# Kernel optimization log

Measured on AMD Instinct MI355X. Metric: run time of the kernel, lower is better.

## Reference

```python
import jax, jax.numpy as jnp
import numpy as np

N, E, L = 20000, 640000, 2
D_IN, D_H, D_FF = 1546, 128, 512  # in_channels, heads*out_channels, ff_dim
EPS = 1e-5
SLOPE = 0.01  # LeakyReLU default negative slope


def layer_norm(x, g, b):
    m = x.mean(-1, keepdims=True)
    v = ((x - m) ** 2).mean(-1, keepdims=True)
    return (x - m) / jnp.sqrt(v + EPS) * g + b


def setup_inputs() -> dict:
    key = jax.random.key(0)
    ks = iter(jax.random.split(key, 40))
    f32 = jnp.float32
    def w(shape, scale=0.05):
        return jax.random.normal(next(ks), shape, dtype=f32) * scale
    inp = {
        "x": jax.random.normal(next(ks), (N, D_IN), dtype=f32),
        "edge_index": jax.random.randint(next(ks), (2, E), 0, N, dtype=jnp.int64),
        "edge_attr": jax.random.normal(next(ks), (E, D_H), dtype=f32),
        # per-layer TransformerConv params, stacked over L layers
        "Wq": w((L, D_IN, D_H)), "bq": jnp.zeros((L, D_H), f32),
        "Wk": w((L, D_IN, D_H)), "bk": jnp.zeros((L, D_H), f32),
        "Wv": w((L, D_IN, D_H)), "bv": jnp.zeros((L, D_H), f32),
        "Wr": w((L, D_IN, D_H)), "br": jnp.zeros((L, D_H), f32),
        "Whi": w((L, D_IN, D_H)), "Whj": w((L, D_IN, D_H)),
        # per-layer FFMLP params
        "W1": w((L, D_H, D_FF)), "b1": jnp.zeros((L, D_FF), f32),
        "W2": w((L, D_FF, D_H)), "b2": jnp.zeros((L, D_H), f32),
        "g1": jnp.ones((L, D_H), f32), "be1": jnp.zeros((L, D_H), f32),
        "g2": jnp.ones((L, D_H), f32), "be2": jnp.zeros((L, D_H), f32),
        # shared linear 128->1546 and final linear2 1546->128
        "linW": w((D_H, D_IN)), "linb": jnp.zeros((D_IN,), f32),
        "lin2W": w((D_IN, D_H)), "lin2b": jnp.zeros((D_H,), f32),
    }
    return inp


def reference(x, edge_index, edge_attr, Wq, bq, Wk, bk, Wv, bv, Wr, br,
              Whi, Whj, W1, b1, W2, b2, g1, be1, g2, be2,
              linW, linb, lin2W, lin2b):
    src = edge_index[0]  # j (source)
    dst = edge_index[1]  # i (target)
    for l in range(L):
        q = x @ Wq[l] + bq[l]          # [N, D_H]
        k = x @ Wk[l] + bk[l]
        v = x @ Wv[l] + bv[l]
        hi = x @ Whi[l]
        hj = x @ Whj[l]
        # edge gate (uses raw edge_attr, matching original forward)
        gate = jax.nn.sigmoid(edge_attr + hi[src] + hj[dst])      # [E, D_H]
        # per-edge scalar attention, softmax over ALL edges (dim=0, as in source)
        attn = jnp.sum(q[dst] * k[src], axis=-1, keepdims=True)   # [E, 1]
        attn = jax.nn.softmax(attn, axis=0)
        msg = attn * v[src] * gate                                 # [E, D_H]
        aggr = jax.ops.segment_sum(msg, dst, num_segments=N)       # [N, D_H]
        h = aggr + x @ Wr[l] + br[l]   # root weight, concat=False -> no out_proj
        # FFMLP (pre-norm residual on normalized input)
        ss = layer_norm(h, g1[l], be1[l])
        ss2 = jax.nn.relu(ss @ W1[l] + b1[l]) @ W2[l] + b2[l]
        h = layer_norm(ss + ss2, g2[l], be2[l])
        x = h @ linW + linb            # shared 128 -> 1546
    x = jax.nn.leaky_relu(x @ lin2W + lin2b, SLOPE)
    return x
```

## Files before the change

### kernel.cpp

```cpp
#include <hip/hip_runtime.h>
#include <cfloat>
#include <cmath>

#define NN 20000
#define EE 640000
#define DIN 1546
#define KIN 1568
#define DH 128
#define DFF 512
#define NL 2
#define NPROJ 768
#define NB (NN / 4)

typedef unsigned short ushort_t;
typedef __attribute__((ext_vector_type(8))) short short8;
typedef __attribute__((ext_vector_type(8))) unsigned short ushort8;
typedef __attribute__((ext_vector_type(4))) float floatx4;

__device__ inline ushort_t f2bf(float f) {
  unsigned u = __float_as_uint(f);
  unsigned r = (u + 0x7FFF + ((u >> 16) & 1)) >> 16;
  return (ushort_t)r;
}
__device__ inline float bflo(unsigned u) { return __uint_as_float(u << 16); }
__device__ inline float bfhi(unsigned u) { return __uint_as_float(u & 0xFFFF0000u); }

__global__ __launch_bounds__(256) void gemm_bf16(
    const ushort_t* __restrict__ A, int lda,
    const ushort_t* __restrict__ Bt, int ldb,
    const float* __restrict__ bias, void* __restrict__ Cv, int ldc,
    int M, int Nstore, int K, int act, int out_bf16)
{
  __shared__ ushort_t As[4 * 1032];
  __shared__ ushort_t Bs[4 * 1032];
  const int tid = threadIdx.x;
  const int wave = tid >> 6, lane = tid & 63;
  const int bm = blockIdx.x * 128, bn = blockIdx.y * 128;
  const int wm = (wave >> 1) * 64, wn = (wave & 1) * 64;
  const int frow = lane & 15, kq = lane >> 4;

  floatx4 acc[4][4];
  #pragma unroll
  for (int i = 0; i < 4; ++i)
    #pragma unroll
    for (int j = 0; j < 4; ++j) acc[i][j] = (floatx4){0.f, 0.f, 0.f, 0.f};

  const int srow = tid >> 2, skc = tid & 3;
  const int ar0 = min(bm + srow, M - 1);
  const int ar1 = min(bm + srow + 64, M - 1);
  const ushort_t* Ap0 = A + (size_t)ar0 * lda + skc * 8;
  const ushort_t* Ap1 = A + (size_t)ar1 * lda + skc * 8;
  const ushort_t* Bp0 = Bt + (size_t)(bn + srow) * ldb + skc * 8;
  const ushort_t* Bp1 = Bt + (size_t)(bn + srow + 64) * ldb + skc * 8;
  ushort_t* Aw0 = As + skc * 1032 + srow * 8;
  ushort_t* Aw1 = As + skc * 1032 + (srow + 64) * 8;
  ushort_t* Bw0 = Bs + skc * 1032 + srow * 8;
  ushort_t* Bw1 = Bs + skc * 1032 + (srow + 64) * 8;

  for (int k0 = 0; k0 < K; k0 += 32) {
    ushort8 a0 = *(const ushort8*)Ap0; Ap0 += 32;
    ushort8 a1 = *(const ushort8*)Ap1; Ap1 += 32;
    ushort8 b0 = *(const ushort8*)Bp0; Bp0 += 32;
    ushort8 b1 = *(const ushort8*)Bp1; Bp1 += 32;
    __syncthreads();
    *(ushort8*)Aw0 = a0; *(ushort8*)Aw1 = a1;
    *(ushort8*)Bw0 = b0; *(ushort8*)Bw1 = b1;
    __syncthreads();
    short8 af[4], bfv[4];
    #pragma unroll
    for (int i = 0; i < 4; ++i)
      af[i] = *(const short8*)(As + kq * 1032 + (wm + i * 16 + frow) * 8);
    #pragma unroll
    for (int j = 0; j < 4; ++j)
      bfv[j] = *(const short8*)(Bs + kq * 1032 + (wn + j * 16 + frow) * 8);
    #pragma unroll
    for (int i = 0; i < 4; ++i)
      #pragma unroll
      for (int j = 0; j < 4; ++j)
        acc[i][j] = __builtin_amdgcn_mfma_f32_16x16x32_bf16(af[i], bfv[j], acc[i][j], 0, 0, 0);
  }

  const int rq = (lane >> 4) * 4;
  #pragma unroll
  for (int j = 0; j < 4; ++j) {
    int col = bn + wn + j * 16 + frow;
    if (col >= Nstore) continue;
    float bb = bias ? bias[col] : 0.f;
    #pragma unroll
    for (int i = 0; i < 4; ++i) {
      #pragma unroll
      for (int r = 0; r < 4; ++r) {
        int row = bm + wm + i * 16 + rq + r;
        if (row >= M) continue;
        float v = acc[i][j][r] + bb;
        if (act == 1) v = fmaxf(v, 0.f);
        else if (act == 2) v = v > 0.f ? v : 0.01f * v;
        if (out_bf16) ((ushort_t*)Cv)[(size_t)row * ldc + col] = f2bf(v);
        else          ((float*)Cv)[(size_t)row * ldc + col] = v;
      }
    }
  }
}

__global__ __launch_bounds__(256) void gemm_ff2_ln(
    const ushort_t* __restrict__ A,
    const ushort_t* __restrict__ Bt,
    const float* __restrict__ bias,
    const float* __restrict__ ss,
    const float* __restrict__ g, const float* __restrict__ b,
    ushort_t* __restrict__ Yb, int M)
{
  __shared__ ushort_t As[4 * 1032];
  __shared__ ushort_t Bs[4 * 1032];
  __shared__ float vrow[128][130];
  const int tid = threadIdx.x;
  const int wave = tid >> 6, lane = tid & 63;
  const int bm = blockIdx.x * 128;
  const int wm = (wave >> 1) * 64, wn = (wave & 1) * 64;
  const int frow = lane & 15, kq = lane >> 4;

  floatx4 acc[4][4];
  #pragma unroll
  for (int i = 0; i < 4; ++i)
    #pragma unroll
    for (int j = 0; j < 4; ++j) acc[i][j] = (floatx4){0.f, 0.f, 0.f, 0.f};

  const int srow = tid >> 2, skc = tid & 3;
  const ushort_t* Ap0 = A + (size_t)min(bm + srow, M - 1) * DFF + skc * 8;
  const ushort_t* Ap1 = A + (size_t)min(bm + srow + 64, M - 1) * DFF + skc * 8;
  const ushort_t* Bp0 = Bt + (size_t)srow * DFF + skc * 8;
  const ushort_t* Bp1 = Bt + (size_t)(srow + 64) * DFF + skc * 8;
  ushort_t* Aw0 = As + skc * 1032 + srow * 8;
  ushort_t* Aw1 = As + skc * 1032 + (srow + 64) * 8;
  ushort_t* Bw0 = Bs + skc * 1032 + srow * 8;
  ushort_t* Bw1 = Bs + skc * 1032 + (srow + 64) * 8;

  for (int k0 = 0; k0 < DFF; k0 += 32) {
    ushort8 a0 = *(const ushort8*)Ap0; Ap0 += 32;
    ushort8 a1 = *(const ushort8*)Ap1; Ap1 += 32;
    ushort8 b0 = *(const ushort8*)Bp0; Bp0 += 32;
    ushort8 b1 = *(const ushort8*)Bp1; Bp1 += 32;
    __syncthreads();
    *(ushort8*)Aw0 = a0; *(ushort8*)Aw1 = a1;
    *(ushort8*)Bw0 = b0; *(ushort8*)Bw1 = b1;
    __syncthreads();
    short8 af[4], bfv[4];
    #pragma unroll
    for (int i = 0; i < 4; ++i)
      af[i] = *(const short8*)(As + kq * 1032 + (wm + i * 16 + frow) * 8);
    #pragma unroll
    for (int j = 0; j < 4; ++j)
      bfv[j] = *(const short8*)(Bs + kq * 1032 + (wn + j * 16 + frow) * 8);
    #pragma unroll
    for (int i = 0; i < 4; ++i)
      #pragma unroll
      for (int j = 0; j < 4; ++j)
        acc[i][j] = __builtin_amdgcn_mfma_f32_16x16x32_bf16(af[i], bfv[j], acc[i][j], 0, 0, 0);
  }

  const int rq = (lane >> 4) * 4;
  #pragma unroll
  for (int j = 0; j < 4; ++j) {
    int col = wn + j * 16 + frow;
    float bb = bias[col];
    #pragma unroll
    for (int i = 0; i < 4; ++i) {
      #pragma unroll
      for (int r = 0; r < 4; ++r) {
        int row = wm + i * 16 + rq + r;
        int grow = bm + row;
        float v = acc[i][j][r] + bb;
        if (grow < M) v += ss[(size_t)grow * DH + col];
        vrow[row][col] = v;
      }
    }
  }
  __syncthreads();

  float2 gg = *(const float2*)(g + lane * 2);
  float2 bbv = *(const float2*)(b + lane * 2);
  for (int rr = 0; rr < 32; ++rr) {
    int row = wave * 32 + rr;
    int grow = bm + row;
    if (grow >= M) break;
    float x0 = vrow[row][lane * 2], x1 = vrow[row][lane * 2 + 1];
    float s = x0 + x1;
    #pragma unroll
    for (int m = 32; m >= 1; m >>= 1) s += __shfl_xor(s, m);
    float mean = s * (1.f / 128.f);
    float dx = x0 - mean, dy = x1 - mean;
    float v = dx * dx + dy * dy;
    #pragma unroll
    for (int m = 32; m >= 1; m >>= 1) v += __shfl_xor(v, m);
    float rstd = rsqrtf(v * (1.f / 128.f) + 1e-5f);
    float o0 = dx * rstd * gg.x + bbv.x;
    float o1 = dy * rstd * gg.y + bbv.y;
    ushort_t* pp = Yb + (size_t)grow * DH + lane * 2;
    pp[0] = f2bf(o0); pp[1] = f2bf(o1);
  }
}

__global__ __launch_bounds__(256) void convert_x_kernel(
    const float* __restrict__ x, ushort_t* __restrict__ xb)
{
  const unsigned CPR = KIN / 8;
  unsigned gid = blockIdx.x * 256 + threadIdx.x;
  if (gid >= (unsigned)NN * CPR) return;
  unsigned row = gid / CPR;
  unsigned c8 = (gid - row * CPR) * 8;
  const float* xr = x + (size_t)row * DIN;
  ushort8 o;
  #pragma unroll
  for (int j = 0; j < 8; ++j)
    o[j] = (c8 + j < DIN) ? f2bf(xr[c8 + j]) : (ushort_t)0;
  *(ushort8*)(xb + (size_t)row * KIN + c8) = o;
}

__global__ __launch_bounds__(256) void pack6t_kernel(
    const float* __restrict__ Wq, const float* __restrict__ Wk,
    const float* __restrict__ Wv, const float* __restrict__ Wr,
    const float* __restrict__ Whi, const float* __restrict__ Whj,
    ushort_t* __restrict__ Wt6)
{
  __shared__ float tile[32][33];
  const int k0 = blockIdx.x * 32;
  const int n0 = blockIdx.y * 32;
  const float* Ws[6] = {Wq, Wk, Wv, Wr, Whi, Whj};
  const float* W = Ws[n0 >> 7];
  const int c0 = n0 & 127;
  const int tc = threadIdx.x & 31, tr = threadIdx.x >> 5;
  #pragma unroll
  for (int r = tr; r < 32; r += 8) {
    int k = k0 + r;
    tile[r][tc] = (k < DIN) ? W[(size_t)k * DH + c0 + tc] : 0.f;
  }
  __syncthreads();
  #pragma unroll
  for (int n = tr; n < 32; n += 8)
    Wt6[(size_t)(n0 + n) * KIN + k0 + tc] = f2bf(tile[tc][n]);
}

__global__ void pack_small_kernel(
    const float* __restrict__ W1, const float* __restrict__ W2,
    const float* __restrict__ bq, const float* __restrict__ bk,
    const float* __restrict__ bv, const float* __restrict__ br,
    ushort_t* __restrict__ W1t0, ushort_t* __restrict__ W1t1,
    ushort_t* __restrict__ W2t0, ushort_t* __restrict__ W2t1,
    float* __restrict__ bias768)
{
  const int y = blockIdx.y;
  const int tid = threadIdx.x;
  if (y < 1024) {
    int l = y >> 9, n = y & 511;
    const float* src = W1 + (size_t)l * DH * DFF;
    ushort_t* dst = l ? W1t1 : W1t0;
    if (tid < DH) dst[(size_t)n * DH + tid] = f2bf(src[(size_t)tid * DFF + n]);
  } else if (y < 1280) {
    int l = (y - 1024) >> 7, n = (y - 1024) & 127;
    const float* src = W2 + (size_t)l * DFF * DH;
    ushort_t* dst = l ? W2t1 : W2t0;
    for (int k = tid; k < DFF; k += 256)
      dst[(size_t)n * DFF + k] = f2bf(src[(size_t)k * DH + n]);
  } else {
    int n = (y - 1280) * 256 + tid;
    if (n < NPROJ) {
      int which = n >> 7, c = n & 127;
      float v = 0.f;
      if (which == 0) v = bq[c]; else if (which == 1) v = bk[c];
      else if (which == 2) v = bv[c]; else if (which == 3) v = br[c];
      bias768[n] = v;
    }
  }
}

__global__ __launch_bounds__(256) void combine_all_kernel(
    const float* __restrict__ Wq, const float* __restrict__ Wk,
    const float* __restrict__ Wv, const float* __restrict__ Wr,
    const float* __restrict__ Whi, const float* __restrict__ Whj,
    const float* __restrict__ bq, const float* __restrict__ bk,
    const float* __restrict__ bv, const float* __restrict__ br,
    const float* __restrict__ lin2W, const float* __restrict__ lin2b,
    const float* __restrict__ linW, const float* __restrict__ linb,
    ushort_t* __restrict__ Pc, float* __restrict__ bc,
    ushort_t* __restrict__ Pf, float* __restrict__ bf_out)
{
  const int j = threadIdx.x >> 7;
  const int k = threadIdx.x & 127;
  const bool six = blockIdx.x < (NPROJ / 2);
  const int n = six ? blockIdx.x * 2 + j : (blockIdx.x - NPROJ / 2) * 2 + j;
  const float* Ws[6] = {Wq, Wk, Wv, Wr, Whi, Whj};
  const float* W = six ? Ws[n >> 7] : lin2W;
  const int col = six ? (n & 127) : n;
  __shared__ float wcol[2][DIN];
  for (int d = k; d < DIN; d += 128)
    wcol[j][d] = W[(size_t)d * DH + col];
  __syncthreads();
  const float* lr = linW + (size_t)k * DIN;
  float acc = 0.f;
  #pragma unroll 4
  for (int d = 0; d < DIN; d += 2) {
    float2 lv = *(const float2*)(lr + d);
    acc = fmaf(wcol[j][d], lv.x, acc);
    acc = fmaf(wcol[j][d + 1], lv.y, acc);
  }
  if (six) Pc[(size_t)n * DH + k] = f2bf(acc);
  else     Pf[(size_t)n * DH + k] = f2bf(acc);
  float bs = 0.f;
  for (int d = k; d < DIN; d += 128) bs += linb[d] * wcol[j][d];
  #pragma unroll
  for (int m = 32; m >= 1; m >>= 1) bs += __shfl_xor(bs, m);
  __shared__ float red[4];
  if ((threadIdx.x & 63) == 0) red[threadIdx.x >> 6] = bs;
  __syncthreads();
  if (k == 0) {
    float tot = red[j * 2] + red[j * 2 + 1];
    if (six) {
      int which = n >> 7, c = n & 127;
      float b0 = 0.f;
      if (which == 0) b0 = bq[c]; else if (which == 1) b0 = bk[c];
      else if (which == 2) b0 = bv[c]; else if (which == 3) b0 = br[c];
      bc[n] = b0 + tot;
    } else {
      bf_out[n] = lin2b[n] + tot;
    }
  }
}

__global__ void hist_kernel(const int* __restrict__ ei, int* __restrict__ counts) {
  int e = blockIdx.x * 256 + threadIdx.x;
  if (e < EE) atomicAdd(&counts[ei[EE + e]], 1);
}

__global__ __launch_bounds__(1024) void scan_kernel(const int* __restrict__ counts,
                                                    int* __restrict__ offsets,
                                                    int* __restrict__ cursor) {
  __shared__ int sums[1024];
  const int t = threadIdx.x;
  const int PER = 20;
  int base = t * PER;
  int loc[PER]; int s = 0;
  #pragma unroll
  for (int i = 0; i < PER; ++i) {
    int idx = base + i;
    int c = (idx < NN) ? counts[idx] : 0;
    loc[i] = s; s += c;
  }
  sums[t] = s;
  __syncthreads();
  for (int d = 1; d < 1024; d <<= 1) {
    int v = (t >= d) ? sums[t - d] : 0;
    __syncthreads();
    sums[t] += v;
    __syncthreads();
  }
  int pre = (t > 0) ? sums[t - 1] : 0;
  #pragma unroll
  for (int i = 0; i < PER; ++i) {
    int idx = base + i;
    if (idx < NN) { offsets[idx] = pre + loc[i]; cursor[idx] = pre + loc[i]; }
  }
  if (t == 0) offsets[NN] = sums[1023];
}

__global__ void scatter_kernel(const int* __restrict__ ei, int* __restrict__ cursor,
                               int* __restrict__ csrc, int* __restrict__ cea) {
  int e = blockIdx.x * 256 + threadIdx.x;
  if (e < EE) {
    int src = ei[e];
    int p = atomicAdd(&cursor[ei[EE + e]], 1);
    csrc[p] = src;
    cea[p] = e;
  }
}

__global__ __launch_bounds__(256) void attn_logits_csr(
    const int* __restrict__ offsets, const int* __restrict__ csrc,
    const ushort_t* __restrict__ qkv, float* __restrict__ s_csr,
    float* __restrict__ mb, float* __restrict__ zb)
{
  const int node = blockIdx.x * 4 + (threadIdx.x >> 6);
  const int lane = threadIdx.x & 63;
  const int sub = lane & 31, hh = lane >> 5;
  float m = -FLT_MAX, z = 0.f;
  if (node < NN) {
    const int off = offsets[node];
    const int deg = offsets[node + 1] - off;
    uint2 qu = *(const uint2*)(qkv + (size_t)node * NPROJ + sub * 4);
    float q0 = bflo(qu.x), q1 = bfhi(qu.x), q2 = bflo(qu.y), q3 = bfhi(qu.y);
    for (int t = hh; t < deg; t += 2) {
      int pos = off + t;
      int src = csrc[pos];
      uint2 ku = *(const uint2*)(qkv + (size_t)src * NPROJ + DH + sub * 4);
      float d = q0 * bflo(ku.x) + q1 * bfhi(ku.x) + q2 * bflo(ku.y) + q3 * bfhi(ku.y);
      #pragma unroll
      for (int mm = 16; mm >= 1; mm >>= 1) d += __shfl_xor(d, mm);
      if (sub == 0) s_csr[pos] = d;
      if (d <= m) z += __expf(d - m);
      else { z = z * __expf(m - d) + 1.f; m = d; }
    }
  }
  {
    float mo = __shfl_xor(m, 32), zo = __shfl_xor(z, 32);
    float mn = fmaxf(m, mo);
    z = z * __expf(m - mn) + zo * __expf(mo - mn);
    m = mn;
  }
  __shared__ float ms[4], zs[4];
  if (lane == 0) { ms[threadIdx.x >> 6] = m; zs[threadIdx.x >> 6] = z; }
  __syncthreads();
  if (threadIdx.x == 0) {
    float M4 = fmaxf(fmaxf(ms[0], ms[1]), fmaxf(ms[2], ms[3]));
    float Z4 = zs[0] * __expf(ms[0] - M4) + zs[1] * __expf(ms[1] - M4)
             + zs[2] * __expf(ms[2] - M4) + zs[3] * __expf(ms[3] - M4);
    mb[blockIdx.x] = M4; zb[blockIdx.x] = Z4;
  }
}

__global__ __launch_bounds__(1024) void smreduce_kernel(
    const float* __restrict__ mb, const float* __restrict__ zb,
    float* __restrict__ scal)
{
  const int t = threadIdx.x;
  float m = -FLT_MAX, z = 0.f;
  for (int i = t; i < NB; i += 1024) {
    float mi = mb[i], zi = zb[i];
    float mn = fmaxf(m, mi);
    z = z * __expf(m - mn) + zi * __expf(mi - mn);
    m = mn;
  }
  #pragma unroll
  for (int s = 32; s >= 1; s >>= 1) {
    float mo = __shfl_xor(m, s), zo = __shfl_xor(z, s);
    float mn = fmaxf(m, mo);
    z = z * __expf(m - mn) + zo * __expf(mo - mn);
    m = mn;
  }
  __shared__ float ms[16], zs[16];
  if ((t & 63) == 0) { ms[t >> 6] = m; zs[t >> 6] = z; }
  __syncthreads();
  if (t == 0) {
    float M = ms[0], Z = zs[0];
    for (int i = 1; i < 16; ++i) {
      float mn = fmaxf(M, ms[i]);
      Z = Z * __expf(M - mn) + zs[i] * __expf(ms[i] - mn);
      M = mn;
    }
    scal[0] = M; scal[1] = Z;
  }
}

__global__ __launch_bounds__(256) void aggregate_ln_kernel(
    const int* __restrict__ offsets, const int* __restrict__ csrc,
    const int* __restrict__ cea, const float* __restrict__ s_csr,
    const float* __restrict__ scal, const ushort_t* __restrict__ qkv,
    const float* __restrict__ ea,
    const float* __restrict__ g, const float* __restrict__ b,
    float* __restrict__ ss, ushort_t* __restrict__ ssbf)
{
  const int node = blockIdx.x * 4 + (threadIdx.x >> 6);
  const int lane = threadIdx.x & 63;
  if (node >= NN) return;
  const int off = offsets[node];
  const int deg = offsets[node + 1] - off;
  const float M = scal[0];
  const float invZ = 1.f / scal[1];
  const ushort_t* bd = qkv + (size_t)node * NPROJ;
  unsigned hjp = *(const unsigned*)(bd + 640 + lane * 2);
  unsigned rp  = *(const unsigned*)(bd + 384 + lane * 2);
  const float hj0 = bflo(hjp), hj1 = bfhi(hjp);
  float a0 = bflo(rp), a1 = bfhi(rp);
  for (int b0 = 0; b0 < deg; b0 += 64) {
    int t = b0 + lane;
    bool valid = t < deg;
    int pos = off + (valid ? t : 0);
    int sL = valid ? csrc[pos] : 0;
    int eL = valid ? cea[pos] : 0;
    float pL = valid ? __expf(s_csr[pos] - M) * invZ : 0.f;
    int cnt = min(64, deg - b0);
    for (int u = 0; u < cnt; ++u) {
      int e = __shfl(eL, u);
      int src = __shfl(sL, u);
      float p = __shfl(pL, u);
      const ushort_t* bs = qkv + (size_t)src * NPROJ;
      unsigned vv = *(const unsigned*)(bs + 256 + lane * 2);
      unsigned hv = *(const unsigned*)(bs + 512 + lane * 2);
      float2 eav = *(const float2*)(ea + (size_t)e * DH + lane * 2);
      float g0 = 1.f / (1.f + __expf(-(eav.x + bflo(hv) + hj0)));
      float g1 = 1.f / (1.f + __expf(-(eav.y + bfhi(hv) + hj1)));
      a0 = fmaf(p * bflo(vv), g0, a0);
      a1 = fmaf(p * bfhi(vv), g1, a1);
    }
  }
  float s = a0 + a1;
  #pragma unroll
  for (int m = 32; m >= 1; m >>= 1) s += __shfl_xor(s, m);
  float mean = s * (1.f / 128.f);
  float dx = a0 - mean, dy = a1 - mean;
  float v = dx * dx + dy * dy;
  #pragma unroll
  for (int m = 32; m >= 1; m >>= 1) v += __shfl_xor(v, m);
  float rstd = rsqrtf(v * (1.f / 128.f) + 1e-5f);
  float2 gg = *(const float2*)(g + lane * 2);
  float2 bb = *(const float2*)(b + lane * 2);
  float o0 = dx * rstd * gg.x + bb.x;
  float o1 = dy * rstd * gg.y + bb.y;
  *(float2*)(ss + (size_t)node * DH + lane * 2) = make_float2(o0, o1);
  ushort_t* pp = ssbf + (size_t)node * DH + lane * 2;
  pp[0] = f2bf(o0); pp[1] = f2bf(o1);
}

extern "C" void kernel_launch(void* const* d_in, const int* in_sizes, int n_in,
                              void* d_out, int out_size, void* d_ws, size_t ws_size,
                              hipStream_t stream)
{
  const float* x_in  = (const float*)d_in[0];
  const int*   ei    = (const int*)d_in[1];
  const float* ea    = (const float*)d_in[2];
  const float* Wq    = (const float*)d_in[3];
  const float* bq    = (const float*)d_in[4];
  const float* Wk    = (const float*)d_in[5];
  const float* bk    = (const float*)d_in[6];
  const float* Wv    = (const float*)d_in[7];
  const float* bv    = (const float*)d_in[8];
  const float* Wr    = (const float*)d_in[9];
  const float* br    = (const float*)d_in[10];
  const float* Whi   = (const float*)d_in[11];
  const float* Whj   = (const float*)d_in[12];
  const float* W1    = (const float*)d_in[13];
  const float* b1    = (const float*)d_in[14];
  const float* W2    = (const float*)d_in[15];
  const float* b2    = (const float*)d_in[16];
  const float* g1    = (const float*)d_in[17];
  const float* be1   = (const float*)d_in[18];
  const float* g2    = (const float*)d_in[19];
  const float* be2   = (const float*)d_in[20];
  const float* linW  = (const float*)d_in[21];
  const float* linb  = (const float*)d_in[22];
  const float* lin2W = (const float*)d_in[23];
  const float* lin2b = (const float*)d_in[24];
  float* out = (float*)d_out;

  char* p = (char*)d_ws;
  auto alloc = [&](size_t bytes) -> void* {
    void* r = (void*)p; p += (bytes + 63) & ~((size_t)63); return r;
  };
  ushort_t* x_bf   = (ushort_t*)alloc((size_t)NN * KIN * 2);
  ushort_t* qkvp   = (ushort_t*)alloc((size_t)NN * NPROJ * 2);
  ushort_t* Wt6    = (ushort_t*)alloc((size_t)NPROJ * KIN * 2);
  ushort_t* W1t0   = (ushort_t*)alloc((size_t)DFF * DH * 2);
  ushort_t* W1t1   = (ushort_t*)alloc((size_t)DFF * DH * 2);
  ushort_t* W2t0   = (ushort_t*)alloc((size_t)DH * DFF * 2);
  ushort_t* W2t1   = (ushort_t*)alloc((size_t)DH * DFF * 2);
  ushort_t* Wc6    = (ushort_t*)alloc((size_t)NPROJ * DH * 2);
  ushort_t* Wcf    = (ushort_t*)alloc((size_t)DH * DH * 2);
  float*    bias768= (float*)alloc(NPROJ * 4);
  float*    bc768  = (float*)alloc(NPROJ * 4);
  float*    bcf    = (float*)alloc(DH * 4);
  float*    s_csr  = (float*)alloc((size_t)EE * 4);
  float*    scal   = (float*)alloc(64);
  int*      counts = (int*)alloc((size_t)NN * 4);
  int*      offsets= (int*)alloc((size_t)(NN + 1) * 4);
  int*      cursor = (int*)alloc((size_t)NN * 4);
  int*      csrc   = (int*)alloc((size_t)EE * 4);
  int*      cea    = (int*)alloc((size_t)EE * 4);
  float*    mb     = (float*)alloc((size_t)NB * 4);
  float*    zb     = (float*)alloc((size_t)NB * 4);
  float*    ss     = (float*)alloc((size_t)NN * DH * 4);
  ushort_t* ssbf   = (ushort_t*)alloc((size_t)NN * DH * 2);
  ushort_t* ff1bf  = (ushort_t*)alloc((size_t)NN * DFF * 2);
  ushort_t* h2bf   = (ushort_t*)alloc((size_t)NN * DH * 2);

  const dim3 blk(256);
  const int MB = (NN + 127) / 128;

  convert_x_kernel<<<dim3((NN * (KIN / 8) + 255) / 256), blk, 0, stream>>>(x_in, x_bf);
  hipMemsetAsync(counts, 0, (size_t)NN * 4, stream);
  hist_kernel<<<dim3(EE / 256), blk, 0, stream>>>(ei, counts);
  scan_kernel<<<dim3(1), dim3(1024), 0, stream>>>(counts, offsets, cursor);
  scatter_kernel<<<dim3(EE / 256), blk, 0, stream>>>(ei, cursor, csrc, cea);
  pack6t_kernel<<<dim3(KIN / 32, NPROJ / 32), blk, 0, stream>>>(
      Wq, Wk, Wv, Wr, Whi, Whj, Wt6);
  pack_small_kernel<<<dim3(1, 1283), blk, 0, stream>>>(
      W1, W2, bq, bk, bv, br, W1t0, W1t1, W2t0, W2t1, bias768);
  const size_t wo1 = (size_t)DIN * DH;
  combine_all_kernel<<<dim3(NPROJ / 2 + DH / 2), blk, 0, stream>>>(
      Wq + wo1, Wk + wo1, Wv + wo1, Wr + wo1, Whi + wo1, Whj + wo1,
      bq + DH, bk + DH, bv + DH, br + DH,
      lin2W, lin2b, linW, linb, Wc6, bc768, Wcf, bcf);

  for (int l = 0; l < NL; ++l) {
    if (l == 0) {
      gemm_bf16<<<dim3(MB, 6), blk, 0, stream>>>(
          x_bf, KIN, Wt6, KIN, bias768, qkvp, NPROJ, NN, NPROJ, KIN, 0, 1);
    } else {
      gemm_bf16<<<dim3(MB, 6), blk, 0, stream>>>(
          h2bf, DH, Wc6, DH, bc768, qkvp, NPROJ, NN, NPROJ, DH, 0, 1);
    }

    attn_logits_csr<<<dim3(NB), blk, 0, stream>>>(offsets, csrc, qkvp, s_csr, mb, zb);
    smreduce_kernel<<<dim3(1), dim3(1024), 0, stream>>>(mb, zb, scal + l * 2);
    aggregate_ln_kernel<<<dim3(NB), blk, 0, stream>>>(
        offsets, csrc, cea, s_csr, scal + l * 2, qkvp, ea,
        g1 + (size_t)l * DH, be1 + (size_t)l * DH, ss, ssbf);

    gemm_bf16<<<dim3(MB, 4), blk, 0, stream>>>(
        ssbf, DH, l ? W1t1 : W1t0, DH, b1 + (size_t)l * DFF, ff1bf, DFF, NN, DFF, DH, 1, 1);
    gemm_ff2_ln<<<dim3(MB, 1), blk, 0, stream>>>(
        ff1bf, l ? W2t1 : W2t0, b2 + (size_t)l * DH, ss,
        g2 + (size_t)l * DH, be2 + (size_t)l * DH, h2bf, NN);
  }

  gemm_bf16<<<dim3(MB, 1), blk, 0, stream>>>(
      h2bf, DH, Wcf, DH, bcf, out, DH, NN, DH, DH, 2, 0);
}
```

Baseline: 1.436 ms.

## Fuse attention logits and gated aggregation with online per-node softmax rescaling

Merges the logit pass and the aggregation pass into one edge kernel. It keeps a per-node running max and rescales the accumulated weighted messages online, so each node emits an unnormalized aggregate and its local max. A light follow-up kernel rescales each node by exp(m_node - M)/Z, using the global max and sum, and then applies LayerNorm. This avoids a second gather over k/v/gate/edge_attr and the per-edge logit buffer, at the cost of extra exp and rescale work per edge and an NN×DH float scratch buffer.

```diff
diff --git a/kernel.cpp b/kernel.cpp
--- a/kernel.cpp
+++ b/kernel.cpp
@@ -373,40 +373,72 @@
   }
 }
 
-__global__ __launch_bounds__(256) void attn_logits_csr(
+__global__ __launch_bounds__(256) void edge_fused_kernel(
     const int* __restrict__ offsets, const int* __restrict__ csrc,
-    const ushort_t* __restrict__ qkv, float* __restrict__ s_csr,
+    const int* __restrict__ cea, const ushort_t* __restrict__ qkv,
+    const float* __restrict__ ea,
+    float* __restrict__ Abuf, float* __restrict__ mnode,
     float* __restrict__ mb, float* __restrict__ zb)
 {
-  const int node = blockIdx.x * 4 + (threadIdx.x >> 6);
+  const int wid = threadIdx.x >> 6;
+  const int node = blockIdx.x * 4 + wid;
   const int lane = threadIdx.x & 63;
   const int sub = lane & 31, hh = lane >> 5;
   float m = -FLT_MAX, z = 0.f;
-  if (node < NN) {
-    const int off = offsets[node];
-    const int deg = offsets[node + 1] - off;
-    uint2 qu = *(const uint2*)(qkv + (size_t)node * NPROJ + sub * 4);
-    float q0 = bflo(qu.x), q1 = bfhi(qu.x), q2 = bflo(qu.y), q3 = bfhi(qu.y);
-    for (int t = hh; t < deg; t += 2) {
-      int pos = off + t;
-      int src = csrc[pos];
-      uint2 ku = *(const uint2*)(qkv + (size_t)src * NPROJ + DH + sub * 4);
-      float d = q0 * bflo(ku.x) + q1 * bfhi(ku.x) + q2 * bflo(ku.y) + q3 * bfhi(ku.y);
-      #pragma unroll
-      for (int mm = 16; mm >= 1; mm >>= 1) d += __shfl_xor(d, mm);
-      if (sub == 0) s_csr[pos] = d;
-      if (d <= m) z += __expf(d - m);
-      else { z = z * __expf(m - d) + 1.f; m = d; }
-    }
+  float a0 = 0.f, a1 = 0.f, a2 = 0.f, a3 = 0.f;
+
+  const int off = offsets[node];
+  const int deg = offsets[node + 1] - off;
+  const ushort_t* bd = qkv + (size_t)node * NPROJ;
+  uint2 qu = *(const uint2*)(bd + sub * 4);
+  const float q0 = bflo(qu.x), q1 = bfhi(qu.x), q2 = bflo(qu.y), q3 = bfhi(qu.y);
+  uint2 hjv = *(const uint2*)(bd + 640 + sub * 4);
+  const float hj0 = bflo(hjv.x), hj1 = bfhi(hjv.x), hj2 = bflo(hjv.y), hj3 = bfhi(hjv.y);
+
+  for (int t = hh; t < deg; t += 2) {
+    int pos = off + t;
+    int src = csrc[pos];
+    int e   = cea[pos];
+    const ushort_t* bs = qkv + (size_t)src * NPROJ;
+    uint2 ku = *(const uint2*)(bs + DH  + sub * 4);
+    uint2 vu = *(const uint2*)(bs + 256 + sub * 4);
+    uint2 hu = *(const uint2*)(bs + 512 + sub * 4);
+    float4 ev = *(const float4*)(ea + (size_t)e * DH + sub * 4);
+    float d = q0 * bflo(ku.x) + q1 * bfhi(ku.x) + q2 * bflo(ku.y) + q3 * bfhi(ku.y);
+    #pragma unroll
+    for (int mm = 16; mm >= 1; mm >>= 1) d += __shfl_xor(d, mm);
+    float mn = fmaxf(m, d);
+    float sc = __expf(m - mn);
+    float w  = __expf(d - mn);
+    z = z * sc + w;
+    a0 *= sc; a1 *= sc; a2 *= sc; a3 *= sc;
+    m = mn;
+    float g0 = 1.f / (1.f + __expf(-(ev.x + bflo(hu.x) + hj0)));
+    float g1 = 1.f / (1.f + __expf(-(ev.y + bfhi(hu.x) + hj1)));
+    float g2v = 1.f / (1.f + __expf(-(ev.z + bflo(hu.y) + hj2)));
+    float g3 = 1.f / (1.f + __expf(-(ev.w + bfhi(hu.y) + hj3)));
+    a0 = fmaf(w * bflo(vu.x), g0, a0);
+    a1 = fmaf(w * bfhi(vu.x), g1, a1);
+    a2 = fmaf(w * bflo(vu.y), g2v, a2);
+    a3 = fmaf(w * bfhi(vu.y), g3, a3);
   }
   {
     float mo = __shfl_xor(m, 32), zo = __shfl_xor(z, 32);
+    float b0o = __shfl_xor(a0, 32), b1o = __shfl_xor(a1, 32);
+    float b2o = __shfl_xor(a2, 32), b3o = __shfl_xor(a3, 32);
     float mn = fmaxf(m, mo);
-    z = z * __expf(m - mn) + zo * __expf(mo - mn);
+    float ws = __expf(m - mn), wo = __expf(mo - mn);
+    a0 = a0 * ws + b0o * wo; a1 = a1 * ws + b1o * wo;
+    a2 = a2 * ws + b2o * wo; a3 = a3 * ws + b3o * wo;
+    z = z * ws + zo * wo;
     m = mn;
   }
+  if (hh == 0) {
+    *(float4*)(Abuf + (size_t)node * DH + sub * 4) = make_float4(a0, a1, a2, a3);
+    if (sub == 0) mnode[node] = m;
+  }
   __shared__ float ms[4], zs[4];
-  if (lane == 0) { ms[threadIdx.x >> 6] = m; zs[threadIdx.x >> 6] = z; }
+  if (lane == 0) { ms[wid] = m; zs[wid] = z; }
   __syncthreads();
   if (threadIdx.x == 0) {
     float M4 = fmaxf(fmaxf(ms[0], ms[1]), fmaxf(ms[2], ms[3]));
@@ -449,48 +481,22 @@
   }
 }
 
-__global__ __launch_bounds__(256) void aggregate_ln_kernel(
-    const int* __restrict__ offsets, const int* __restrict__ csrc,
-    const int* __restrict__ cea, const float* __restrict__ s_csr,
+__global__ __launch_bounds__(256) void scale_ln_kernel(
+    const float* __restrict__ Abuf, const float* __restrict__ mnode,
     const float* __restrict__ scal, const ushort_t* __restrict__ qkv,
-    const float* __restrict__ ea,
     const float* __restrict__ g, const float* __restrict__ b,
     float* __restrict__ ss, ushort_t* __restrict__ ssbf)
 {
   const int node = blockIdx.x * 4 + (threadIdx.x >> 6);
   const int lane = threadIdx.x & 63;
   if (node >= NN) return;
-  const int off = offsets[node];
-  const int deg = offsets[node + 1] - off;
   const float M = scal[0];
   const float invZ = 1.f / scal[1];
-  const ushort_t* bd = qkv + (size_t)node * NPROJ;
-  unsigned hjp = *(const unsigned*)(bd + 640 + lane * 2);
-  unsigned rp  = *(const unsigned*)(bd + 384 + lane * 2);
-  const float hj0 = bflo(hjp), hj1 = bfhi(hjp);
-  float a0 = bflo(rp), a1 = bfhi(rp);
-  for (int b0 = 0; b0 < deg; b0 += 64) {
-    int t = b0 + lane;
-    bool valid = t < deg;
-    int pos = off + (valid ? t : 0);
-    int sL = valid ? csrc[pos] : 0;
-    int eL = valid ? cea[pos] : 0;
-    float pL = valid ? __expf(s_csr[pos] - M) * invZ : 0.f;
-    int cnt = min(64, deg - b0);
-    for (int u = 0; u < cnt; ++u) {
-      int e = __shfl(eL, u);
-      int src = __shfl(sL, u);
-      float p = __shfl(pL, u);
-      const ushort_t* bs = qkv + (size_t)src * NPROJ;
-      unsigned vv = *(const unsigned*)(bs + 256 + lane * 2);
-      unsigned hv = *(const unsigned*)(bs + 512 + lane * 2);
-      float2 eav = *(const float2*)(ea + (size_t)e * DH + lane * 2);
-      float g0 = 1.f / (1.f + __expf(-(eav.x + bflo(hv) + hj0)));
-      float g1 = 1.f / (1.f + __expf(-(eav.y + bfhi(hv) + hj1)));
-      a0 = fmaf(p * bflo(vv), g0, a0);
-      a1 = fmaf(p * bfhi(vv), g1, a1);
-    }
-  }
+  const float gam = __expf(mnode[node] - M) * invZ;
+  float2 A = *(const float2*)(Abuf + (size_t)node * DH + lane * 2);
+  unsigned rp = *(const unsigned*)(qkv + (size_t)node * NPROJ + 384 + lane * 2);
+  float a0 = fmaf(gam, A.x, bflo(rp));
+  float a1 = fmaf(gam, A.y, bfhi(rp));
   float s = a0 + a1;
   #pragma unroll
   for (int m = 32; m >= 1; m >>= 1) s += __shfl_xor(s, m);
@@ -556,7 +562,6 @@
   float*    bias768= (float*)alloc(NPROJ * 4);
   float*    bc768  = (float*)alloc(NPROJ * 4);
   float*    bcf    = (float*)alloc(DH * 4);
-  float*    s_csr  = (float*)alloc((size_t)EE * 4);
   float*    scal   = (float*)alloc(64);
   int*      counts = (int*)alloc((size_t)NN * 4);
   int*      offsets= (int*)alloc((size_t)(NN + 1) * 4);
@@ -565,6 +570,8 @@
   int*      cea    = (int*)alloc((size_t)EE * 4);
   float*    mb     = (float*)alloc((size_t)NB * 4);
   float*    zb     = (float*)alloc((size_t)NB * 4);
+  float*    Abuf   = (float*)alloc((size_t)NN * DH * 4);
+  float*    mnode  = (float*)alloc((size_t)NN * 4);
   float*    ss     = (float*)alloc((size_t)NN * DH * 4);
   ushort_t* ssbf   = (ushort_t*)alloc((size_t)NN * DH * 2);
   ushort_t* ff1bf  = (ushort_t*)alloc((size_t)NN * DFF * 2);
@@ -597,10 +604,11 @@
           h2bf, DH, Wc6, DH, bc768, qkvp, NPROJ, NN, NPROJ, DH, 0, 1);
     }
 
-    attn_logits_csr<<<dim3(NB), blk, 0, stream>>>(offsets, csrc, qkvp, s_csr, mb, zb);
+    edge_fused_kernel<<<dim3(NB), blk, 0, stream>>>(
+        offsets, csrc, cea, qkvp, ea, Abuf, mnode, mb, zb);
     smreduce_kernel<<<dim3(1), dim3(1024), 0, stream>>>(mb, zb, scal + l * 2);
-    aggregate_ln_kernel<<<dim3(NB), blk, 0, stream>>>(
-        offsets, csrc, cea, s_csr, scal + l * 2, qkvp, ea,
+    scale_ln_kernel<<<dim3(NB), blk, 0, stream>>>(
+        Abuf, mnode, scal + l * 2, qkvp,
         g1 + (size_t)l * DH, be1 + (size_t)l * DH, ss, ssbf);
 
     gemm_bf16<<<dim3(MB, 4), blk, 0, stream>>>(
```

New measurement: 1.381 ms. 3.8% less time.
